# Performance work log

Measured on AMD Instinct MI355X. Metric: run time of the kernel, lower is better.

## Reference

```python
import jax, jax.numpy as jnp
import numpy as np

NUM_EDGES = 10000
NUM_PATHS = 30000
MAX_LEN = 16
LINK_DIM = 128
PATH_DIM = 128


def setup_inputs() -> dict:
    key = jax.random.key(0)
    k0, k1, k2, k3, k4, k5, k6, k7 = jax.random.split(key, 8)
    inputs = jax.random.normal(k0, (NUM_EDGES, LINK_DIM), dtype=jnp.float32)
    # every path has exactly MAX_LEN hops -> unique (path, pos) scatter indices
    idx = jnp.repeat(jnp.arange(NUM_PATHS, dtype=jnp.int64), MAX_LEN)
    seqs = jnp.tile(jnp.arange(MAX_LEN, dtype=jnp.int64), NUM_PATHS)
    paths = jax.random.randint(k1, (NUM_PATHS * MAX_LEN,), 0, NUM_EDGES).astype(jnp.int64)
    # GRU params (Keras GRUCell, reset_after=True): kernel [D,3U], recurrent [U,3U], two bias rows
    s_in = 1.0 / np.sqrt(LINK_DIM)
    s_h = 1.0 / np.sqrt(PATH_DIM)
    kernel = jax.random.uniform(k2, (LINK_DIM, 3 * PATH_DIM), minval=-s_in, maxval=s_in, dtype=jnp.float32)
    rec_kernel = jax.random.uniform(k3, (PATH_DIM, 3 * PATH_DIM), minval=-s_h, maxval=s_h, dtype=jnp.float32)
    bias_i = jnp.zeros((3 * PATH_DIM,), dtype=jnp.float32)
    bias_r = jnp.zeros((3 * PATH_DIM,), dtype=jnp.float32)
    wq = jax.random.uniform(k4, (PATH_DIM, PATH_DIM), minval=-s_h, maxval=s_h, dtype=jnp.float32)
    wk = jax.random.uniform(k5, (PATH_DIM, PATH_DIM), minval=-s_h, maxval=s_h, dtype=jnp.float32)
    wv = jax.random.uniform(k6, (PATH_DIM, PATH_DIM), minval=-s_h, maxval=s_h, dtype=jnp.float32)
    return {"inputs": inputs, "paths": paths, "idx": idx, "seqs": seqs,
            "kernel": kernel, "rec_kernel": rec_kernel, "bias_i": bias_i, "bias_r": bias_r,
            "wq": wq, "wk": wk, "wv": wv}


def _gru_scan(link_inputs, kernel, rec_kernel, bias_i, bias_r):
    # link_inputs: [P, L, D] -> hidden_states [P, L, U], last_state [P, U]
    U = rec_kernel.shape[0]
    P = link_inputs.shape[0]
    xs = jnp.transpose(link_inputs, (1, 0, 2))  # [L, P, D]

    def step(h, x):
        xm = x @ kernel + bias_i          # [P, 3U]
        hm = h @ rec_kernel + bias_r      # [P, 3U]  (reset_after=True)
        xz, xr, xh = xm[:, :U], xm[:, U:2 * U], xm[:, 2 * U:]
        hz, hr, hh = hm[:, :U], hm[:, U:2 * U], hm[:, 2 * U:]
        z = jax.nn.sigmoid(xz + hz)
        r = jax.nn.sigmoid(xr + hr)
        cand = jnp.tanh(xh + r * hh)
        h_new = z * h + (1.0 - z) * cand
        return h_new, h_new

    h0 = jnp.zeros((P, U), dtype=link_inputs.dtype)
    last, hs = jax.lax.scan(step, h0, xs)
    return jnp.transpose(hs, (1, 0, 2)), last  # [P, L, U], [P, U]


def reference(inputs, paths, idx, seqs, kernel, rec_kernel, bias_i, bias_r, wq, wk, wv):
    h_tild = inputs[paths]  # gather: [P*L, D]
    link_inputs = jnp.zeros((NUM_PATHS, MAX_LEN, LINK_DIM), dtype=inputs.dtype)
    link_inputs = link_inputs.at[idx, seqs].set(h_tild)  # scatter_nd
    hidden_states, last_state = _gru_scan(link_inputs, kernel, rec_kernel, bias_i, bias_r)
    key = jnp.einsum('plu,uv->plv', hidden_states, wk)
    query = last_state @ wq                     # [P, U]
    value = jnp.einsum('plu,uv->plv', hidden_states, wv)
    att = jnp.einsum('plv,pv->pl', key, query)  # raw scores, no softmax (faithful)
    context = jnp.einsum('pl,plv->pv', att, value)[:, None, :]  # [P, 1, U]
    return context
```

## Files before the change

kernel.cpp:

```cpp
#include <hip/hip_runtime.h>


#define NUM_PATHS 30000
#define T 16
#define NTILES 1875
#define NPAIRS 938

typedef float f32x4 __attribute__((ext_vector_type(4)));
typedef short bf16x8 __attribute__((ext_vector_type(8)));

__device__ __forceinline__ short f2bf(float f) {
    union { float f; unsigned u; } v; v.f = f;
    return (short)((v.u + 0x8000u) >> 16);
}
__device__ __forceinline__ float bf2f(short s) {
    union { unsigned u; float f; } v; v.u = ((unsigned)(unsigned short)s) << 16;
    return v.f;
}
__device__ __forceinline__ float fsig(float x) {
    return __builtin_amdgcn_rcpf(1.0f + __expf(-x));
}
__device__ __forceinline__ float ftanhf_(float x) {
    return 1.0f - 2.0f * __builtin_amdgcn_rcpf(1.0f + __expf(2.0f * x));
}

#define GRU_T 12288
#define QK_T 16384
#define WV_T 2048
#define TAB_C 160000
__global__ void prep_kernel(const float* __restrict__ inputs,
                            const float* __restrict__ Wx, const float* __restrict__ Wr,
                            const float* __restrict__ wq, const float* __restrict__ wk,
                            const float* __restrict__ wv,
                            short* __restrict__ tab, short* __restrict__ wpk) {
    int id = blockIdx.x * 256 + threadIdx.x;
    if (id < GRU_T) {
        int f = id >> 9, rem = id & 511;
        int w = rem >> 6, lane = rem & 63;
        int quad = lane >> 4, c16 = lane & 15;
        int col = 16 * w + c16;
        short o[8];
        #pragma unroll
        for (int j = 0; j < 8; ++j) {
            float v;
            if (f < 16) {
                int k = (f & 7) * 32 + quad * 8 + j;
                int cc = col + ((f < 8) ? 0 : 128);
                v = (k < 128) ? Wx[k * 384 + cc] : Wr[(k - 128) * 384 + cc];
            } else {
                int k = ((f - 16) & 3) * 32 + quad * 8 + j;
                v = (f < 20) ? Wx[k * 384 + 256 + col] : Wr[k * 384 + 256 + col];
            }
            o[j] = f2bf(v);
        }
        *(bf16x8*)&wpk[id * 8] = *(bf16x8*)o;
        return;
    }
    if (id < GRU_T + QK_T) {
        int t2 = id - GRU_T;
        int j = t2 & 7, lane = (t2 >> 3) & 63, w = (t2 >> 9) & 7, kc = t2 >> 12;
        int quad = lane >> 4, c16 = lane & 15, col = 16 * w + c16;
        int k = kc * 32 + quad * 8 + j;
        const float* qr = wq + k * 128;
        const float* kr = wk + col * 128;
        float s = 0.f;
        #pragma unroll 8
        for (int vv = 0; vv < 128; ++vv) s += qr[vv] * kr[vv];
        short hi = f2bf(s);
        wpk[(((24 + kc) * 8 + w) * 64 + lane) * 8 + j] = hi;
        wpk[(((28 + kc) * 8 + w) * 64 + lane) * 8 + j] = f2bf(s - bf2f(hi));
        return;
    }
    if (id < GRU_T + QK_T + WV_T) {
        int t2 = id - GRU_T - QK_T;
        int lane = t2 & 63, w = (t2 >> 6) & 7, kc = t2 >> 9;
        int quad = lane >> 4, c16 = lane & 15, col = 16 * w + c16;
        short hi8[8], lo8[8];
        #pragma unroll
        for (int j = 0; j < 8; ++j) {
            float v = wv[(kc * 32 + quad * 8 + j) * 128 + col];
            hi8[j] = f2bf(v);
            lo8[j] = f2bf(v - bf2f(hi8[j]));
        }
        *(bf16x8*)&wpk[(((32 + kc) * 8 + w) * 64 + lane) * 8] = *(bf16x8*)hi8;
        *(bf16x8*)&wpk[(((36 + kc) * 8 + w) * 64 + lane) * 8] = *(bf16x8*)lo8;
        return;
    }
    int cid = id - (GRU_T + QK_T + WV_T);
    if (cid < TAB_C) {
        float4 a = *(const float4*)&inputs[cid * 8];
        float4 b = *(const float4*)&inputs[cid * 8 + 4];
        short o[8] = {f2bf(a.x), f2bf(a.y), f2bf(a.z), f2bf(a.w),
                      f2bf(b.x), f2bf(b.y), f2bf(b.z), f2bf(b.w)};
        *(bf16x8*)&tab[cid * 8] = *(bf16x8*)o;
    }
}

#define MFMA(a, b, c) __builtin_amdgcn_mfma_f32_16x16x32_bf16((a), (b), (c), 0, 0, 0)

#define ROWS 136
#define HSLOT 2184

__global__ __launch_bounds__(512, 2) void path_emb_kernel(
    const short* __restrict__ tab, const int* __restrict__ paths,
    const short* __restrict__ wpk,
    const float* __restrict__ bias_i, const float* __restrict__ bias_r,
    float* __restrict__ out)
{
    __shared__ __align__(16) short s_hist[2][16][HSLOT];
    __shared__ __align__(16) short s_xb[2][2][T * ROWS];
    __shared__ float s_att[2][16][20];

    const int tid  = threadIdx.x;
    const int w    = tid >> 6;
    const int lane = tid & 63;
    const int quad = lane >> 4;
    const int c16  = lane & 15;
    const int ucol = 16 * w + c16;
    const int st   = tid >> 8;
    const int rid  = tid & 255;
    const int srow = rid >> 4;
    const int schunk = (rid & 15) * 8;

    const float bz  = bias_i[ucol] + bias_r[ucol];
    const float brr = bias_i[128 + ucol] + bias_r[128 + ucol];
    const float bxh = bias_i[256 + ucol];
    const float bhh = bias_r[256 + ucol];

    bf16x8 Ball[24];
    #pragma unroll
    for (int f = 0; f < 24; ++f)
        Ball[f] = *(const bf16x8*)&wpk[((f * 8 + w) * 64 + lane) * 8];

    for (int pi = blockIdx.x; pi < NPAIRS; pi += gridDim.x) {
        const int tA = 2 * pi;
        const int tB = (2 * pi + 1 < NTILES) ? 2 * pi + 1 : NTILES - 1;
        const int p0A = tA * T, p0B = tB * T;
        const int spr = ((st ? p0B : p0A) + srow) * 16;

        __syncthreads();
        {
            int e = paths[spr];
            *(bf16x8*)&s_xb[st][0][srow * ROWS + schunk] = *(const bf16x8*)&tab[e * 128 + schunk];
        }

        float hA[4] = {0.f, 0.f, 0.f, 0.f}, hB[4] = {0.f, 0.f, 0.f, 0.f};

        for (int t = 0; t < 16; ++t) {
            __syncthreads();

            if (t < 15) {
                int e = paths[spr + t + 1];
                *(bf16x8*)&s_xb[st][(t + 1) & 1][srow * ROWS + schunk] =
                    *(const bf16x8*)&tab[e * 128 + schunk];
            }

            bf16x8 axA[4], axB[4], ahA[4], ahB[4];
            #pragma unroll
            for (int kc = 0; kc < 4; ++kc) {
                axA[kc] = *(const bf16x8*)&s_xb[0][t & 1][c16 * ROWS + kc * 32 + quad * 8];
                axB[kc] = *(const bf16x8*)&s_xb[1][t & 1][c16 * ROWS + kc * 32 + quad * 8];
            }
            if (t > 0) {
                #pragma unroll
                for (int kc = 0; kc < 4; ++kc) {
                    ahA[kc] = *(const bf16x8*)&s_hist[0][t - 1][c16 * ROWS + kc * 32 + quad * 8];
                    ahB[kc] = *(const bf16x8*)&s_hist[1][t - 1][c16 * ROWS + kc * 32 + quad * 8];
                }
            }

            f32x4 azA = {bz, bz, bz, bz},    azB = azA;
            f32x4 arA = {brr, brr, brr, brr}, arB = arA;
            f32x4 acxA = {bxh, bxh, bxh, bxh}, acxB = acxA;
            f32x4 achA = {bhh, bhh, bhh, bhh}, achB = achA;

            #pragma unroll
            for (int kc = 0; kc < 4; ++kc) {
                azA  = MFMA(axA[kc], Ball[kc],      azA);
                azB  = MFMA(axB[kc], Ball[kc],      azB);
                arA  = MFMA(axA[kc], Ball[8 + kc],  arA);
                arB  = MFMA(axB[kc], Ball[8 + kc],  arB);
                acxA = MFMA(axA[kc], Ball[16 + kc], acxA);
                acxB = MFMA(axB[kc], Ball[16 + kc], acxB);
            }
            if (t > 0) {
                #pragma unroll
                for (int kc = 0; kc < 4; ++kc) {
                    azA  = MFMA(ahA[kc], Ball[4 + kc],  azA);
                    azB  = MFMA(ahB[kc], Ball[4 + kc],  azB);
                    arA  = MFMA(ahA[kc], Ball[12 + kc], arA);
                    arB  = MFMA(ahB[kc], Ball[12 + kc], arB);
                    achA = MFMA(ahA[kc], Ball[20 + kc], achA);
                    achB = MFMA(ahB[kc], Ball[20 + kc], achB);
                }
            }

            #pragma unroll
            for (int r = 0; r < 4; ++r) {
                float z    = fsig(azA[r]);
                float rr   = fsig(arA[r]);
                float cand = ftanhf_(acxA[r] + rr * achA[r]);
                hA[r] = cand + z * (hA[r] - cand);
                s_hist[0][t][(quad * 4 + r) * ROWS + ucol] = f2bf(hA[r]);
            }
            #pragma unroll
            for (int r = 0; r < 4; ++r) {
                float z    = fsig(azB[r]);
                float rr   = fsig(arB[r]);
                float cand = ftanhf_(acxB[r] + rr * achB[r]);
                hB[r] = cand + z * (hB[r] - cand);
                s_hist[1][t][(quad * 4 + r) * ROWS + ucol] = f2bf(hB[r]);
            }
        }

        #pragma unroll
        for (int r = 0; r < 4; ++r) {
            float hf = hA[r]; short hi = f2bf(hf);
            s_xb[0][0][(quad * 4 + r) * ROWS + ucol] = f2bf(hf - bf2f(hi));
            hf = hB[r]; hi = f2bf(hf);
            s_xb[1][0][(quad * 4 + r) * ROWS + ucol] = f2bf(hf - bf2f(hi));
        }
        __syncthreads();

        f32x4 uA = {0.f, 0.f, 0.f, 0.f}, uB = uA;
        #pragma unroll
        for (int kc = 0; kc < 4; ++kc) {
            bf16x8 bqh = *(const bf16x8*)&wpk[(((24 + kc) * 8 + w) * 64 + lane) * 8];
            bf16x8 bql = *(const bf16x8*)&wpk[(((28 + kc) * 8 + w) * 64 + lane) * 8];
            bf16x8 AhA = *(const bf16x8*)&s_hist[0][15][c16 * ROWS + kc * 32 + quad * 8];
            bf16x8 AlA = *(const bf16x8*)&s_xb[0][0][c16 * ROWS + kc * 32 + quad * 8];
            bf16x8 AhB = *(const bf16x8*)&s_hist[1][15][c16 * ROWS + kc * 32 + quad * 8];
            bf16x8 AlB = *(const bf16x8*)&s_xb[1][0][c16 * ROWS + kc * 32 + quad * 8];
            uA = MFMA(AhA, bqh, uA); uA = MFMA(AhA, bql, uA); uA = MFMA(AlA, bqh, uA);
            uB = MFMA(AhB, bqh, uB); uB = MFMA(AhB, bql, uB); uB = MFMA(AlB, bqh, uB);
        }
        __syncthreads();

        #pragma unroll
        for (int r = 0; r < 4; ++r) {
            int off = (quad * 4 + r) * ROWS + ucol;
            float v = uA[r]; short hi = f2bf(v);
            s_xb[0][0][off] = hi; s_xb[0][1][off] = f2bf(v - bf2f(hi));
            v = uB[r]; hi = f2bf(v);
            s_xb[1][0][off] = hi; s_xb[1][1][off] = f2bf(v - bf2f(hi));
        }
        __syncthreads();

        {
            int et = tid >> 8, p = (tid >> 4) & 15, l = tid & 15;
            const short* uh = &s_xb[et][0][p * ROWS];
            const short* ul = &s_xb[et][1][p * ROWS];
            const short* hh = &s_hist[et][l][p * ROWS];
            float a = 0.f;
            #pragma unroll
            for (int u8 = 0; u8 < 128; u8 += 8) {
                bf16x8 vh = *(const bf16x8*)&uh[u8];
                bf16x8 vl = *(const bf16x8*)&ul[u8];
                bf16x8 vt = *(const bf16x8*)&hh[u8];
                #pragma unroll
                for (int j = 0; j < 8; ++j)
                    a += (bf2f(vh[j]) + bf2f(vl[j])) * bf2f(vt[j]);
            }
            s_att[et][p][l] = a;
        }
        __syncthreads();

        {
            int et = tid >> 8, p = (tid >> 4) & 15, v0 = (tid & 15) * 8;
            float ctx[8];
            #pragma unroll
            for (int j = 0; j < 8; ++j) ctx[j] = 0.f;
            #pragma unroll
            for (int l = 0; l < 16; ++l) {
                float al = s_att[et][p][l];
                bf16x8 hv = *(const bf16x8*)&s_hist[et][l][p * ROWS + v0];
                #pragma unroll
                for (int j = 0; j < 8; ++j) ctx[j] += al * bf2f(hv[j]);
            }
            #pragma unroll
            for (int j = 0; j < 8; ++j) {
                short hi = f2bf(ctx[j]);
                s_xb[et][0][p * ROWS + v0 + j] = hi;
                s_xb[et][1][p * ROWS + v0 + j] = f2bf(ctx[j] - bf2f(hi));
            }
        }
        __syncthreads();

        f32x4 oA = {0.f, 0.f, 0.f, 0.f}, oB = oA;
        #pragma unroll
        for (int kc = 0; kc < 4; ++kc) {
            bf16x8 bwh = *(const bf16x8*)&wpk[(((32 + kc) * 8 + w) * 64 + lane) * 8];
            bf16x8 bwl = *(const bf16x8*)&wpk[(((36 + kc) * 8 + w) * 64 + lane) * 8];
            bf16x8 AhA = *(const bf16x8*)&s_xb[0][0][c16 * ROWS + kc * 32 + quad * 8];
            bf16x8 AlA = *(const bf16x8*)&s_xb[0][1][c16 * ROWS + kc * 32 + quad * 8];
            bf16x8 AhB = *(const bf16x8*)&s_xb[1][0][c16 * ROWS + kc * 32 + quad * 8];
            bf16x8 AlB = *(const bf16x8*)&s_xb[1][1][c16 * ROWS + kc * 32 + quad * 8];
            oA = MFMA(AhA, bwh, oA); oA = MFMA(AhA, bwl, oA); oA = MFMA(AlA, bwh, oA);
            oB = MFMA(AhB, bwh, oB); oB = MFMA(AhB, bwl, oB); oB = MFMA(AlB, bwh, oB);
        }
        #pragma unroll
        for (int r = 0; r < 4; ++r) {
            out[(p0A + quad * 4 + r) * 128 + ucol] = oA[r];
            out[(p0B + quad * 4 + r) * 128 + ucol] = oB[r];
        }
    }
}

extern "C" void kernel_launch(void* const* d_in, const int* in_sizes, int n_in,
                              void* d_out, int out_size, void* d_ws, size_t ws_size,
                              hipStream_t stream) {
    const float* inputs = (const float*)d_in[0];
    const int*   paths  = (const int*)d_in[1];
    const float* wx  = (const float*)d_in[4];
    const float* wr  = (const float*)d_in[5];
    const float* bi  = (const float*)d_in[6];
    const float* br  = (const float*)d_in[7];
    const float* wq  = (const float*)d_in[8];
    const float* wk  = (const float*)d_in[9];
    const float* wvp = (const float*)d_in[10];

    char* ws = (char*)d_ws;
    short* tab = (short*)ws;
    short* wpk = (short*)(ws + 2560000);

    int prep_n = GRU_T + QK_T + WV_T + TAB_C;
    prep_kernel<<<(prep_n + 255) / 256, 256, 0, stream>>>(
        inputs, wx, wr, wq, wk, wvp, tab, wpk);
    path_emb_kernel<<<256, 512, 0, stream>>>(tab, paths, wpk, bi, br, (float*)d_out);
}
```

Measured before the change: 223.4 us.

## Load gathered GRU inputs directly from global into MFMA fragments, skip LDS staging

Drops the double-buffered shared-memory staging of gathered edge rows. Each lane now reads its path indices four at a time as an int4 and loads its bf16 input fragments straight from the global table. The hidden-state MFMAs are reordered to issue before the input MFMAs, so the global-load latency can hide behind recurrent work. This saves LDS traffic and the prefetch writes, but each step now waits on exposed global gather latency with no explicit prefetch, and each row is loaded redundantly by every wave.

```diff
diff --git a/kernel.cpp b/kernel.cpp
--- a/kernel.cpp
+++ b/kernel.cpp
@@ -22,6 +22,9 @@
 }
 __device__ __forceinline__ float ftanhf_(float x) {
     return 1.0f - 2.0f * __builtin_amdgcn_rcpf(1.0f + __expf(2.0f * x));
+}
+__device__ __forceinline__ int sel4(const int4 v, int c) {
+    return (c & 1) ? ((c & 2) ? v.w : v.y) : ((c & 2) ? v.z : v.x);
 }
 
 #define GRU_T 12288
@@ -117,10 +120,6 @@
     const int quad = lane >> 4;
     const int c16  = lane & 15;
     const int ucol = 16 * w + c16;
-    const int st   = tid >> 8;
-    const int rid  = tid & 255;
-    const int srow = rid >> 4;
-    const int schunk = (rid & 15) * 8;
 
     const float bz  = bias_i[ucol] + bias_r[ucol];
     const float brr = bias_i[128 + ucol] + bias_r[128 + ucol];
@@ -136,54 +135,41 @@
         const int tA = 2 * pi;
         const int tB = (2 * pi + 1 < NTILES) ? 2 * pi + 1 : NTILES - 1;
         const int p0A = tA * T, p0B = tB * T;
-        const int spr = ((st ? p0B : p0A) + srow) * 16;
-
-        __syncthreads();
-        {
-            int e = paths[spr];
-            *(bf16x8*)&s_xb[st][0][srow * ROWS + schunk] = *(const bf16x8*)&tab[e * 128 + schunk];
-        }
+        const int prA = p0A + c16;
+        const int prB = p0B + c16;
 
         float hA[4] = {0.f, 0.f, 0.f, 0.f}, hB[4] = {0.f, 0.f, 0.f, 0.f};
+        int4 eiA, eiB;
 
         for (int t = 0; t < 16; ++t) {
             __syncthreads();
 
-            if (t < 15) {
-                int e = paths[spr + t + 1];
-                *(bf16x8*)&s_xb[st][(t + 1) & 1][srow * ROWS + schunk] =
-                    *(const bf16x8*)&tab[e * 128 + schunk];
-            }
-
-            bf16x8 axA[4], axB[4], ahA[4], ahB[4];
+            if ((t & 3) == 0) {
+                eiA = *(const int4*)&paths[prA * 16 + t];
+                eiB = *(const int4*)&paths[prB * 16 + t];
+            }
+            const int eA = sel4(eiA, t & 3), eB = sel4(eiB, t & 3);
+            const short* gA = tab + (long)eA * 128 + quad * 8;
+            const short* gB = tab + (long)eB * 128 + quad * 8;
+            bf16x8 axA[4], axB[4];
             #pragma unroll
             for (int kc = 0; kc < 4; ++kc) {
-                axA[kc] = *(const bf16x8*)&s_xb[0][t & 1][c16 * ROWS + kc * 32 + quad * 8];
-                axB[kc] = *(const bf16x8*)&s_xb[1][t & 1][c16 * ROWS + kc * 32 + quad * 8];
-            }
+                axA[kc] = *(const bf16x8*)(gA + kc * 32);
+                axB[kc] = *(const bf16x8*)(gB + kc * 32);
+            }
+
+            f32x4 azA = {bz, bz, bz, bz},      azB = azA;
+            f32x4 arA = {brr, brr, brr, brr},  arB = arA;
+            f32x4 acxA = {bxh, bxh, bxh, bxh}, acxB = acxA;
+            f32x4 achA = {bhh, bhh, bhh, bhh}, achB = achA;
+
             if (t > 0) {
+                bf16x8 ahA[4], ahB[4];
                 #pragma unroll
                 for (int kc = 0; kc < 4; ++kc) {
                     ahA[kc] = *(const bf16x8*)&s_hist[0][t - 1][c16 * ROWS + kc * 32 + quad * 8];
                     ahB[kc] = *(const bf16x8*)&s_hist[1][t - 1][c16 * ROWS + kc * 32 + quad * 8];
                 }
-            }
-
-            f32x4 azA = {bz, bz, bz, bz},    azB = azA;
-            f32x4 arA = {brr, brr, brr, brr}, arB = arA;
-            f32x4 acxA = {bxh, bxh, bxh, bxh}, acxB = acxA;
-            f32x4 achA = {bhh, bhh, bhh, bhh}, achB = achA;
-
-            #pragma unroll
-            for (int kc = 0; kc < 4; ++kc) {
-                azA  = MFMA(axA[kc], Ball[kc],      azA);
-                azB  = MFMA(axB[kc], Ball[kc],      azB);
-                arA  = MFMA(axA[kc], Ball[8 + kc],  arA);
-                arB  = MFMA(axB[kc], Ball[8 + kc],  arB);
-                acxA = MFMA(axA[kc], Ball[16 + kc], acxA);
-                acxB = MFMA(axB[kc], Ball[16 + kc], acxB);
-            }
-            if (t > 0) {
                 #pragma unroll
                 for (int kc = 0; kc < 4; ++kc) {
                     azA  = MFMA(ahA[kc], Ball[4 + kc],  azA);
@@ -193,6 +179,15 @@
                     achA = MFMA(ahA[kc], Ball[20 + kc], achA);
                     achB = MFMA(ahB[kc], Ball[20 + kc], achB);
                 }
+            }
+            #pragma unroll
+            for (int kc = 0; kc < 4; ++kc) {
+                azA  = MFMA(axA[kc], Ball[kc],      azA);
+                azB  = MFMA(axB[kc], Ball[kc],      azB);
+                arA  = MFMA(axA[kc], Ball[8 + kc],  arA);
+                arB  = MFMA(axB[kc], Ball[8 + kc],  arB);
+                acxA = MFMA(axA[kc], Ball[16 + kc], acxA);
+                acxB = MFMA(axB[kc], Ball[16 + kc], acxB);
             }
 
             #pragma unroll
```

New measurement: 283.8 us. 1.27x slower.

## Precompute per-edge input projections once and gather them inside the GRU loop

Applied to the files above, without the earlier changes.

The input-side GRU projections (x@Wx for the z, r and h gates) are now computed once per edge (10k edges) in a new eprep kernel, not once per path position (480k). The z and r parts are stored as packed bf16 and the h part as fp32. The recurrent kernel then gathers these precomputed values per step, which removes half of its MFMA work and the shared-memory staging of inputs. In exchange it adds an extra kernel launch, a larger gather footprint (8 bytes per unit per edge), and lower precision for the z/r input terms.

```diff
diff --git a/kernel.cpp b/kernel.cpp
--- a/kernel.cpp
+++ b/kernel.cpp
@@ -5,6 +5,7 @@
 #define T 16
 #define NTILES 1875
 #define NPAIRS 938
+#define NEDGES 10000
 
 typedef float f32x4 __attribute__((ext_vector_type(4)));
 typedef short bf16x8 __attribute__((ext_vector_type(8)));
@@ -24,15 +25,15 @@
     return 1.0f - 2.0f * __builtin_amdgcn_rcpf(1.0f + __expf(2.0f * x));
 }
 
+#define MFMA(a, b, c) __builtin_amdgcn_mfma_f32_16x16x32_bf16((a), (b), (c), 0, 0, 0)
+
 #define GRU_T 12288
 #define QK_T 16384
 #define WV_T 2048
-#define TAB_C 160000
-__global__ void prep_kernel(const float* __restrict__ inputs,
-                            const float* __restrict__ Wx, const float* __restrict__ Wr,
+__global__ void prep_kernel(const float* __restrict__ Wx, const float* __restrict__ Wr,
                             const float* __restrict__ wq, const float* __restrict__ wk,
                             const float* __restrict__ wv,
-                            short* __restrict__ tab, short* __restrict__ wpk) {
+                            short* __restrict__ wpk) {
     int id = blockIdx.x * 256 + threadIdx.x;
     if (id < GRU_T) {
         int f = id >> 9, rem = id & 511;
@@ -84,26 +85,54 @@
         }
         *(bf16x8*)&wpk[(((32 + kc) * 8 + w) * 64 + lane) * 8] = *(bf16x8*)hi8;
         *(bf16x8*)&wpk[(((36 + kc) * 8 + w) * 64 + lane) * 8] = *(bf16x8*)lo8;
-        return;
-    }
-    int cid = id - (GRU_T + QK_T + WV_T);
-    if (cid < TAB_C) {
-        float4 a = *(const float4*)&inputs[cid * 8];
-        float4 b = *(const float4*)&inputs[cid * 8 + 4];
+    }
+}
+
+__global__ __launch_bounds__(512) void eprep_kernel(
+    const float* __restrict__ inputs, const short* __restrict__ wpk,
+    uint2* __restrict__ E8) {
+    const int w = threadIdx.x >> 6, lane = threadIdx.x & 63;
+    const int quad = lane >> 4, c16 = lane & 15;
+    const int ucol = 16 * w + c16;
+    const int e0 = blockIdx.x * 16;
+
+    bf16x8 A[4];
+    const float* row = inputs + (e0 + c16) * 128;
+    #pragma unroll
+    for (int kc = 0; kc < 4; ++kc) {
+        float4 a = *(const float4*)&row[kc * 32 + quad * 8];
+        float4 b = *(const float4*)&row[kc * 32 + quad * 8 + 4];
         short o[8] = {f2bf(a.x), f2bf(a.y), f2bf(a.z), f2bf(a.w),
                       f2bf(b.x), f2bf(b.y), f2bf(b.z), f2bf(b.w)};
-        *(bf16x8*)&tab[cid * 8] = *(bf16x8*)o;
-    }
-}
-
-#define MFMA(a, b, c) __builtin_amdgcn_mfma_f32_16x16x32_bf16((a), (b), (c), 0, 0, 0)
+        A[kc] = *(bf16x8*)o;
+    }
+    f32x4 az = {0.f, 0.f, 0.f, 0.f}, ar = az, ax = az;
+    #pragma unroll
+    for (int kc = 0; kc < 4; ++kc) {
+        bf16x8 Bz = *(const bf16x8*)&wpk[(((0 + kc) * 8 + w) * 64 + lane) * 8];
+        bf16x8 Br = *(const bf16x8*)&wpk[(((8 + kc) * 8 + w) * 64 + lane) * 8];
+        bf16x8 Bx = *(const bf16x8*)&wpk[(((16 + kc) * 8 + w) * 64 + lane) * 8];
+        az = MFMA(A[kc], Bz, az);
+        ar = MFMA(A[kc], Br, ar);
+        ax = MFMA(A[kc], Bx, ax);
+    }
+    #pragma unroll
+    for (int r = 0; r < 4; ++r) {
+        unsigned zr = (unsigned)(unsigned short)f2bf(az[r]) |
+                      ((unsigned)(unsigned short)f2bf(ar[r]) << 16);
+        uint2 val;
+        val.x = zr;
+        val.y = __float_as_uint(ax[r]);
+        E8[(e0 + quad * 4 + r) * 128 + ucol] = val;
+    }
+}
 
 #define ROWS 136
 #define HSLOT 2184
 
 __global__ __launch_bounds__(512, 2) void path_emb_kernel(
-    const short* __restrict__ tab, const int* __restrict__ paths,
-    const short* __restrict__ wpk,
+    const int* __restrict__ paths, const short* __restrict__ wpk,
+    const uint2* __restrict__ E8,
     const float* __restrict__ bias_i, const float* __restrict__ bias_r,
     float* __restrict__ out)
 {
@@ -117,100 +146,103 @@
     const int quad = lane >> 4;
     const int c16  = lane & 15;
     const int ucol = 16 * w + c16;
-    const int st   = tid >> 8;
-    const int rid  = tid & 255;
-    const int srow = rid >> 4;
-    const int schunk = (rid & 15) * 8;
 
     const float bz  = bias_i[ucol] + bias_r[ucol];
     const float brr = bias_i[128 + ucol] + bias_r[128 + ucol];
     const float bxh = bias_i[256 + ucol];
     const float bhh = bias_r[256 + ucol];
 
-    bf16x8 Ball[24];
+    bf16x8 Bzh[4], Brh[4], Bhh[4];
     #pragma unroll
-    for (int f = 0; f < 24; ++f)
-        Ball[f] = *(const bf16x8*)&wpk[((f * 8 + w) * 64 + lane) * 8];
+    for (int kc = 0; kc < 4; ++kc) {
+        Bzh[kc] = *(const bf16x8*)&wpk[(((4 + kc)  * 8 + w) * 64 + lane) * 8];
+        Brh[kc] = *(const bf16x8*)&wpk[(((12 + kc) * 8 + w) * 64 + lane) * 8];
+        Bhh[kc] = *(const bf16x8*)&wpk[(((20 + kc) * 8 + w) * 64 + lane) * 8];
+    }
 
     for (int pi = blockIdx.x; pi < NPAIRS; pi += gridDim.x) {
         const int tA = 2 * pi;
         const int tB = (2 * pi + 1 < NTILES) ? 2 * pi + 1 : NTILES - 1;
         const int p0A = tA * T, p0B = tB * T;
-        const int spr = ((st ? p0B : p0A) + srow) * 16;
-
-        __syncthreads();
+
+        float hA[4] = {0.f, 0.f, 0.f, 0.f}, hB[4] = {0.f, 0.f, 0.f, 0.f};
+
+        uint2 Ea[8], Eb[8];
         {
-            int e = paths[spr];
-            *(bf16x8*)&s_xb[st][0][srow * ROWS + schunk] = *(const bf16x8*)&tab[e * 128 + schunk];
-        }
-
-        float hA[4] = {0.f, 0.f, 0.f, 0.f}, hB[4] = {0.f, 0.f, 0.f, 0.f};
-
-        for (int t = 0; t < 16; ++t) {
+            int e0i[8];
+            #pragma unroll
+            for (int i = 0; i < 4; ++i) {
+                e0i[i]     = paths[(p0A + quad * 4 + i) * 16];
+                e0i[4 + i] = paths[(p0B + quad * 4 + i) * 16];
+            }
+            #pragma unroll
+            for (int i = 0; i < 8; ++i) Ea[i] = E8[e0i[i] * 128 + ucol];
+        }
+
+        auto window = [&](int t, uint2* Ecur, uint2* Enext) {
             __syncthreads();
 
             if (t < 15) {
-                int e = paths[spr + t + 1];
-                *(bf16x8*)&s_xb[st][(t + 1) & 1][srow * ROWS + schunk] =
-                    *(const bf16x8*)&tab[e * 128 + schunk];
-            }
-
-            bf16x8 axA[4], axB[4], ahA[4], ahB[4];
-            #pragma unroll
-            for (int kc = 0; kc < 4; ++kc) {
-                axA[kc] = *(const bf16x8*)&s_xb[0][t & 1][c16 * ROWS + kc * 32 + quad * 8];
-                axB[kc] = *(const bf16x8*)&s_xb[1][t & 1][c16 * ROWS + kc * 32 + quad * 8];
-            }
+                int en[8];
+                #pragma unroll
+                for (int i = 0; i < 4; ++i) {
+                    en[i]     = paths[(p0A + quad * 4 + i) * 16 + t + 1];
+                    en[4 + i] = paths[(p0B + quad * 4 + i) * 16 + t + 1];
+                }
+                #pragma unroll
+                for (int i = 0; i < 8; ++i) Enext[i] = E8[en[i] * 128 + ucol];
+            }
+
+            f32x4 azA = {bz, bz, bz, bz},     azB = azA;
+            f32x4 arA = {brr, brr, brr, brr}, arB = arA;
+            f32x4 achA = {bhh, bhh, bhh, bhh}, achB = achA;
+
             if (t > 0) {
+                bf16x8 ahA[4], ahB[4];
                 #pragma unroll
                 for (int kc = 0; kc < 4; ++kc) {
                     ahA[kc] = *(const bf16x8*)&s_hist[0][t - 1][c16 * ROWS + kc * 32 + quad * 8];
                     ahB[kc] = *(const bf16x8*)&s_hist[1][t - 1][c16 * ROWS + kc * 32 + quad * 8];
                 }
-            }
-
-            f32x4 azA = {bz, bz, bz, bz},    azB = azA;
-            f32x4 arA = {brr, brr, brr, brr}, arB = arA;
-            f32x4 acxA = {bxh, bxh, bxh, bxh}, acxB = acxA;
-            f32x4 achA = {bhh, bhh, bhh, bhh}, achB = achA;
-
-            #pragma unroll
-            for (int kc = 0; kc < 4; ++kc) {
-                azA  = MFMA(axA[kc], Ball[kc],      azA);
-                azB  = MFMA(axB[kc], Ball[kc],      azB);
-                arA  = MFMA(axA[kc], Ball[8 + kc],  arA);
-                arB  = MFMA(axB[kc], Ball[8 + kc],  arB);
-                acxA = MFMA(axA[kc], Ball[16 + kc], acxA);
-                acxB = MFMA(axB[kc], Ball[16 + kc], acxB);
-            }
-            if (t > 0) {
                 #pragma unroll
                 for (int kc = 0; kc < 4; ++kc) {
-                    azA  = MFMA(ahA[kc], Ball[4 + kc],  azA);
-                    azB  = MFMA(ahB[kc], Ball[4 + kc],  azB);
-                    arA  = MFMA(ahA[kc], Ball[12 + kc], arA);
-                    arB  = MFMA(ahB[kc], Ball[12 + kc], arB);
-                    achA = MFMA(ahA[kc], Ball[20 + kc], achA);
-                    achB = MFMA(ahB[kc], Ball[20 + kc], achB);
+                    azA  = MFMA(ahA[kc], Bzh[kc], azA);
+                    azB  = MFMA(ahB[kc], Bzh[kc], azB);
+                    arA  = MFMA(ahA[kc], Brh[kc], arA);
+                    arB  = MFMA(ahB[kc], Brh[kc], arB);
+                    achA = MFMA(ahA[kc], Bhh[kc], achA);
+                    achB = MFMA(ahB[kc], Bhh[kc], achB);
                 }
             }
 
             #pragma unroll
             for (int r = 0; r < 4; ++r) {
-                float z    = fsig(azA[r]);
-                float rr   = fsig(arA[r]);
-                float cand = ftanhf_(acxA[r] + rr * achA[r]);
+                float zx = __uint_as_float(Ecur[r].x << 16);
+                float rx = __uint_as_float(Ecur[r].x & 0xffff0000u);
+                float xh = __uint_as_float(Ecur[r].y);
+                float z    = fsig(azA[r] + zx);
+                float rr   = fsig(arA[r] + rx);
+                float cand = ftanhf_(xh + bxh + rr * achA[r]);
                 hA[r] = cand + z * (hA[r] - cand);
                 s_hist[0][t][(quad * 4 + r) * ROWS + ucol] = f2bf(hA[r]);
             }
             #pragma unroll
             for (int r = 0; r < 4; ++r) {
-                float z    = fsig(azB[r]);
-                float rr   = fsig(arB[r]);
-                float cand = ftanhf_(acxB[r] + rr * achB[r]);
+                float zx = __uint_as_float(Ecur[4 + r].x << 16);
+                float rx = __uint_as_float(Ecur[4 + r].x & 0xffff0000u);
+                float xh = __uint_as_float(Ecur[4 + r].y);
+                float z    = fsig(azB[r] + zx);
+                float rr   = fsig(arB[r] + rx);
+                float cand = ftanhf_(xh + bxh + rr * achB[r]);
                 hB[r] = cand + z * (hB[r] - cand);
                 s_hist[1][t][(quad * 4 + r) * ROWS + ucol] = f2bf(hB[r]);
             }
+        };
+
+        #pragma unroll 1
+        for (int t2 = 0; t2 < 8; ++t2) {
+            window(2 * t2,     Ea, Eb);
+            window(2 * t2 + 1, Eb, Ea);
         }
 
         #pragma unroll
@@ -320,11 +352,11 @@
     const float* wvp = (const float*)d_in[10];
 
     char* ws = (char*)d_ws;
-    short* tab = (short*)ws;
-    short* wpk = (short*)(ws + 2560000);
-
-    int prep_n = GRU_T + QK_T + WV_T + TAB_C;
-    prep_kernel<<<(prep_n + 255) / 256, 256, 0, stream>>>(
-        inputs, wx, wr, wq, wk, wvp, tab, wpk);
-    path_emb_kernel<<<256, 512, 0, stream>>>(tab, paths, wpk, bi, br, (float*)d_out);
-}
+    uint2* E8 = (uint2*)ws;
+    short* wpk = (short*)(ws + 10240000);
+
+    int prep_n = GRU_T + QK_T + WV_T;
+    prep_kernel<<<(prep_n + 255) / 256, 256, 0, stream>>>(wx, wr, wq, wk, wvp, wpk);
+    eprep_kernel<<<NEDGES / 16, 512, 0, stream>>>(inputs, wpk, E8);
+    path_emb_kernel<<<256, 512, 0, stream>>>(paths, wpk, E8, bi, br, (float*)d_out);
+}
```

After: 219.8 us. Within noise of the previous version (-1.6%).
